# Kernel optimization log

Hardware: AMD Instinct MI355X
Metric: run time of the kernel (lower is better)

Reference implementation:

```python
import jax, jax.numpy as jnp
import numpy as np

EPS = 1e-8
EPS12 = 1e-12
TAU = 0.2
IOU_THRESHOLD = 0.5
NEG_INF = -1e9

N, C = 8192, 1024
HID, FGD, CLSD = 256, 64, 128


def setup_inputs() -> dict:
    key = jax.random.key(0)
    ks = jax.random.split(key, 16)
    roi_feats = jax.random.normal(ks[0], (N, C), dtype=jnp.float32)
    # labels in {-1 (ignore), 0 (bg), 1..20 (classes)}
    labels = jax.random.randint(ks[1], (N,), 0, 21, dtype=jnp.int64) - 1
    ious = jax.random.uniform(ks[2], (N,), dtype=jnp.float32)
    s = 0.02
    w1f = jax.random.normal(ks[3], (HID, C), dtype=jnp.float32) * s
    b1f = jnp.zeros((HID,), dtype=jnp.float32)
    w2f = jax.random.normal(ks[4], (FGD, HID), dtype=jnp.float32) * s
    b2f = jnp.zeros((FGD,), dtype=jnp.float32)
    w1c = jax.random.normal(ks[5], (HID, C), dtype=jnp.float32) * s
    b1c = jnp.zeros((HID,), dtype=jnp.float32)
    w2c = jax.random.normal(ks[6], (CLSD, HID), dtype=jnp.float32) * s
    b2c = jnp.zeros((CLSD,), dtype=jnp.float32)
    return {"roi_feats": roi_feats, "labels": labels, "ious": ious,
            "w1f": w1f, "b1f": b1f, "w2f": w2f, "b2f": b2f,
            "w1c": w1c, "b1c": b1c, "w2c": w2c, "b2c": b2c}


def _project_normalize(x, w1, b1, w2, b2):
    h = jax.nn.relu(x @ w1.T + b1)
    z = h @ w2.T + b2
    nrm = jnp.linalg.norm(z, axis=1, keepdims=True)  # F.normalize: z / max(||z||, eps)
    return z / jnp.maximum(nrm, EPS)


def _fg_bg_loss(z_fg, fg_mask, ignore_mask, iou_weight):
    n = z_fg.shape[0]
    anchor = fg_mask & ~ignore_mask
    eye = jnp.eye(n, dtype=bool)
    # pos_mask[i,j] = fg_mask[j] & ~ignore[j], self excluded
    pos = (fg_mask & ~ignore_mask)[None, :] & ~eye  # [N,N]
    sim = (z_fg @ z_fg.T) / TAU
    sim_exp = jnp.exp(sim) * (~eye).astype(sim.dtype)
    denom = sim_exp.sum(axis=1)  # [N]
    numer = jnp.sum(jnp.exp(sim) * pos.astype(sim.dtype), axis=1)  # [N]
    n_pos = pos.sum(axis=1)
    loss_i = -jnp.log((numer + EPS) / (denom + EPS))
    valid = anchor & (n_pos > 0)
    w = iou_weight
    num = jnp.sum(jnp.where(valid, loss_i * w, 0.0))
    den = jnp.sum(jnp.where(valid, w, 0.0)) + EPS
    return num / den


def _class_supcon_loss(z_cls, labels, fg_mask, ignore_mask, iou_weight):
    n = z_cls.shape[0]
    anchor = fg_mask & ~ignore_mask
    eye = jnp.eye(n, dtype=bool)
    valid_den = ~eye & ~ignore_mask[None, :]  # [N,N]
    # pos[i,j]: same label, j not ignored, labels[j] != 0, j != i, j valid
    pos = (labels[None, :] == labels[:, None]) & ~ignore_mask[None, :] & (labels[None, :] != 0)
    pos = pos & ~eye & valid_den
    sim = (z_cls @ z_cls.T) / TAU
    logits = jnp.where(valid_den, sim, NEG_INF)
    denom_log = jax.nn.logsumexp(logits, axis=1)  # [N]
    n_pos = pos.sum(axis=1)
    sum_pos = jnp.sum(jnp.where(pos, sim, 0.0), axis=1)
    n_pos_safe = jnp.maximum(n_pos, 1).astype(sim.dtype)
    loss_i = -(sum_pos - n_pos.astype(sim.dtype) * denom_log) / n_pos_safe
    valid = anchor & (n_pos > 0) & valid_den.any(axis=1)
    w = iou_weight
    num = jnp.sum(jnp.where(valid, loss_i * w, 0.0))
    den = jnp.sum(jnp.where(valid, w, 0.0)) + EPS12
    return num / den


def reference(roi_feats, labels, ious, w1f, b1f, w2f, b2f, w1c, b1c, w2c, b2c):
    z_fg = _project_normalize(roi_feats, w1f, b1f, w2f, b2f)
    z_cls = _project_normalize(roi_feats, w1c, b1c, w2c, b2c)
    ignore_mask = labels == -1
    bg_mask = (labels == 0) & ~ignore_mask
    fg_mask = (labels > 0) & ~ignore_mask
    iou_weight = jnp.where(ious > IOU_THRESHOLD, ious, 0.0)
    loss_fg_bg = _fg_bg_loss(z_fg, fg_mask, ignore_mask, iou_weight)
    loss_supcon = _class_supcon_loss(z_cls, labels, fg_mask, ignore_mask, iou_weight)
    # loss_weights = (1.0, 1.0); stacked as [loss_fg_bg, loss_supcon]
    return jnp.stack([loss_fg_bg * 1.0, loss_supcon * 1.0])
```

## Files before the change

kernel.cpp:

```cpp
#include <hip/hip_runtime.h>
#include <hip/hip_bf16.h>
#include <math.h>

#define N_ROI 8192
#define C_IN  1024
#define HIDD  256
#define FGD   64
#define CLSD  128
#define INV_TAU 5.0f

using frag_ab = __attribute__((ext_vector_type(8))) short;
using f32x16  = __attribute__((ext_vector_type(16))) float;

static __device__ __forceinline__ short f32_to_bf16_bits(float f) {
  unsigned u = __builtin_bit_cast(unsigned, f);
  u = (u + 0x7FFFu + ((u >> 16) & 1u)) >> 16;
  return (short)u;
}
static __device__ __forceinline__ float bf16_bits_to_f32(short b) {
  unsigned u = ((unsigned)(unsigned short)b) << 16;
  return __builtin_bit_cast(float, u);
}

__global__ void prep_zero_kernel(float* accum, int* cnt) {
  int t = threadIdx.x;
  if (t < 8) accum[t] = 0.f;
  if (t < 24) cnt[t] = 0;
}

__global__ void prep_stats_kernel(const int* __restrict__ labels,
                                  float* __restrict__ Sfg, float* __restrict__ Pfg,
                                  float* __restrict__ Scls, float* __restrict__ SPc,
                                  float* __restrict__ pfv, float* __restrict__ nimv,
                                  float* __restrict__ ljmv, int* __restrict__ cnt) {
  int i = blockIdx.x * blockDim.x + threadIdx.x;
  if (i >= N_ROI) return;
  Sfg[i] = 0.f; Pfg[i] = 0.f; Scls[i] = 0.f; SPc[i] = 0.f;
  int l = labels[i];
  pfv[i]  = (l > 0)  ? 1.f : 0.f;
  nimv[i] = (l != -1) ? 1.f : 0.f;
  ljmv[i] = (l > 0)  ? (float)l : -7.f;
  int b = l + 1; if (b < 0) b = 0; if (b > 21) b = 21;
  atomicAdd(&cnt[b], 1);
}

__global__ __launch_bounds__(256) void pack_w_kernel(
    const float* __restrict__ w1f, const float* __restrict__ w1c,
    const float* __restrict__ w2f, const float* __restrict__ w2c,
    short* __restrict__ W1pf, short* __restrict__ W1pc,
    short* __restrict__ W2pf, short* __restrict__ W2pc) {
  int b = blockIdx.x;
  const float* src; short* dst; int Ksh; int b0;
  if (b < 128)      { src = w1f; dst = W1pf; Ksh = 10; b0 = 0; }
  else if (b < 256) { src = w1c; dst = W1pc; Ksh = 10; b0 = 128; }
  else if (b < 264) { src = w2f; dst = W2pf; Ksh = 8;  b0 = 256; }
  else              { src = w2c; dst = W2pc; Ksh = 8;  b0 = 264; }
  int K = 1 << Ksh;
  int f = (b - b0) * 256 + threadIdx.x;
  int r = f >> (Ksh - 3);
  int c0 = (f & ((K >> 3) - 1)) << 3;
  float4 v0 = *(const float4*)(src + (size_t)r * K + c0);
  float4 v1 = *(const float4*)(src + (size_t)r * K + c0 + 4);
  union { short s[8]; uint4 v; } o;
  o.s[0] = f32_to_bf16_bits(v0.x); o.s[1] = f32_to_bf16_bits(v0.y);
  o.s[2] = f32_to_bf16_bits(v0.z); o.s[3] = f32_to_bf16_bits(v0.w);
  o.s[4] = f32_to_bf16_bits(v1.x); o.s[5] = f32_to_bf16_bits(v1.y);
  o.s[6] = f32_to_bf16_bits(v1.z); o.s[7] = f32_to_bf16_bits(v1.w);
  ((uint4*)dst)[(size_t)((r >> 5) * (K >> 4) + (c0 >> 4)) * 64 +
                ((c0 >> 3) & 1) * 32 + (r & 31)] = o.v;
}

__global__ __launch_bounds__(256) void gemm1_kernel(
    const float* __restrict__ X,
    const short* __restrict__ W1pf, const short* __restrict__ W1pc,
    const float* __restrict__ b1f, const float* __restrict__ b1c,
    short* __restrict__ Hpf, short* __restrict__ Hpc) {
  __shared__ union {
    short stageA[2][1024];
    short T[4][128 * 36];
  } sm;
  int tid = threadIdx.x, lane = tid & 63, wv = tid >> 6;
  int Mb = blockIdx.x;
  const short* Wp = (wv >> 1) ? W1pc : W1pf;
  const float* b1 = (wv >> 1) ? b1c  : b1f;
  short*       Hp = (wv >> 1) ? Hpc  : Hpf;
  const uint4* Wv4 = (const uint4*)Wp;
  int arow = tid >> 3;
  int ac4  = tid & 7;
  const float* Xp = X + (size_t)(Mb * 32 + arow) * C_IN + ac4 * 4;
  int aslot = ((ac4 >> 2) * 64 + ((ac4 >> 1) & 1) * 32 + arow) * 8 + (ac4 & 1) * 4;

  float4 av;
  frag_ab breg[2][8];
  f32x16 acc[4];
  #pragma unroll
  for (int nt = 0; nt < 4; ++nt)
    #pragma unroll
    for (int q = 0; q < 16; ++q) acc[nt][q] = 0.f;

  auto loadA = [&](int c) { av = *(const float4*)(Xp + c * 32); };
  auto loadB = [&](int c, int s) {
    #pragma unroll
    for (int kci = 0; kci < 2; ++kci)
      #pragma unroll
      for (int nt = 0; nt < 4; ++nt)
        breg[s][kci * 4 + nt] =
            *(const frag_ab*)&Wv4[(size_t)(((wv & 1) * 4 + nt) * 64 + c * 2 + kci) * 64 + lane];
  };
  auto storeA = [&](int buf) {
    *(short4*)&sm.stageA[buf][aslot] =
        make_short4(f32_to_bf16_bits(av.x), f32_to_bf16_bits(av.y),
                    f32_to_bf16_bits(av.z), f32_to_bf16_bits(av.w));
  };
  auto domfma = [&](int buf, int bank) {
    frag_ab a0 = *(const frag_ab*)&sm.stageA[buf][(0 * 64 + lane) * 8];
    frag_ab a1 = *(const frag_ab*)&sm.stageA[buf][(1 * 64 + lane) * 8];
    #pragma unroll
    for (int nt = 0; nt < 4; ++nt)
      acc[nt] = __builtin_amdgcn_mfma_f32_32x32x16_bf16(a0, breg[bank][nt], acc[nt], 0, 0, 0);
    #pragma unroll
    for (int nt = 0; nt < 4; ++nt)
      acc[nt] = __builtin_amdgcn_mfma_f32_32x32x16_bf16(a1, breg[bank][4 + nt], acc[nt], 0, 0, 0);
  };

  loadA(0); loadB(0, 0); storeA(0);
  __syncthreads();
  for (int c = 0; c < 32; c += 2) {
    if (c + 1 < 32) { loadA(c + 1); loadB(c + 1, 1); }
    domfma(0, 0);
    if (c + 1 < 32) storeA(1);
    __syncthreads();
    if (c + 2 < 32) { loadA(c + 2); loadB(c + 2, 0); }
    domfma(1, 1);
    if (c + 2 < 32) storeA(0);
    __syncthreads();
  }
  int cl31 = lane & 31, h = lane >> 5;
  short* T = sm.T[wv];
  #pragma unroll
  for (int nt = 0; nt < 4; ++nt) {
    int colLocal = nt * 32 + cl31;
    float bb = b1[(wv & 1) * 128 + colLocal];
    #pragma unroll
    for (int g = 0; g < 4; ++g) {
      float x0 = fmaxf(acc[nt][g * 4 + 0] + bb, 0.f);
      float x1 = fmaxf(acc[nt][g * 4 + 1] + bb, 0.f);
      float x2 = fmaxf(acc[nt][g * 4 + 2] + bb, 0.f);
      float x3 = fmaxf(acc[nt][g * 4 + 3] + bb, 0.f);
      *(short4*)&T[colLocal * 36 + 4 * h + 8 * g] =
          make_short4(f32_to_bf16_bits(x0), f32_to_bf16_bits(x1),
                      f32_to_bf16_bits(x2), f32_to_bf16_bits(x3));
    }
  }
  __syncthreads();
  uint4* Hv4 = (uint4*)Hp;
  #pragma unroll
  for (int k = 0; k < 8; ++k) {
    union { short s[8]; uint4 v; } o;
    int c0 = k * 16 + h * 8;
    #pragma unroll
    for (int e = 0; e < 8; ++e) o.s[e] = T[(c0 + e) * 36 + cl31];
    Hv4[(size_t)(Mb * 16 + (wv & 1) * 8 + k) * 64 + h * 32 + cl31] = o.v;
  }
}

template<int D>
__device__ __forceinline__ void gemm2_head(
    const short* __restrict__ Hp, const short* __restrict__ W2p,
    const float* __restrict__ b2, short* __restrict__ Zr,
    float* __restrict__ tii, short* __restrict__ T, int gt) {
  int lane = threadIdx.x & 63;
  const frag_ab* Hv = (const frag_ab*)Hp;
  const frag_ab* Wv = (const frag_ab*)W2p;
  constexpr int NT = D / 32;
  frag_ab a[16];
  #pragma unroll
  for (int kc = 0; kc < 16; ++kc) a[kc] = Hv[(size_t)(gt * 16 + kc) * 64 + lane];
  f32x16 acc[NT];
  #pragma unroll
  for (int j = 0; j < NT; ++j)
    #pragma unroll
    for (int q = 0; q < 16; ++q) acc[j][q] = 0.f;
  #pragma unroll
  for (int kc = 0; kc < 16; ++kc)
    #pragma unroll
    for (int j = 0; j < NT; ++j)
      acc[j] = __builtin_amdgcn_mfma_f32_32x32x16_bf16(a[kc], Wv[(j * 16 + kc) * 64 + lane], acc[j], 0, 0, 0);
  int c = lane & 31, h = lane >> 5;
  float bb[NT];
  #pragma unroll
  for (int j = 0; j < NT; ++j) bb[j] = b2[j * 32 + c];
  float s1[16];
  #pragma unroll
  for (int r = 0; r < 16; ++r) {
    s1[r] = 0.f;
    #pragma unroll
    for (int j = 0; j < NT; ++j) {
      float v = acc[j][r] + bb[j];
      s1[r] += v * v;
    }
  }
  #pragma unroll
  for (int r = 0; r < 16; ++r)
    #pragma unroll
    for (int m = 1; m < 32; m <<= 1) s1[r] += __shfl_xor(s1[r], m);
  float s2[16];
  #pragma unroll
  for (int r = 0; r < 16; ++r) s2[r] = 0.f;
  #pragma unroll
  for (int j = 0; j < NT; ++j) {
    int cl = j * 32 + c;
    #pragma unroll
    for (int g = 0; g < 4; ++g) {
      short q0, q1, q2, q3;
      #pragma unroll
      for (int e = 0; e < 4; ++e) {
        int r = g * 4 + e;
        float sc = 1.f / fmaxf(sqrtf(s1[r]), 1e-8f);
        short qb = f32_to_bf16_bits((acc[j][r] + bb[j]) * sc);
        float zf = bf16_bits_to_f32(qb);
        s2[r] += zf * zf;
        if (e == 0) q0 = qb; else if (e == 1) q1 = qb; else if (e == 2) q2 = qb; else q3 = qb;
      }
      *(short4*)&T[cl * 36 + 4 * h + 8 * g] = make_short4(q0, q1, q2, q3);
    }
  }
  #pragma unroll
  for (int r = 0; r < 16; ++r)
    #pragma unroll
    for (int m = 1; m < 32; m <<= 1) s2[r] += __shfl_xor(s2[r], m);
  if (c == 0) {
    #pragma unroll
    for (int r = 0; r < 16; ++r)
      tii[gt * 32 + (r & 3) + 8 * (r >> 2) + 4 * h] = s2[r];
  }
  __syncthreads();
  uint4* Zv = (uint4*)Zr;
  #pragma unroll
  for (int k = 0; k < D / 16; ++k) {
    int c0 = (2 * k + h) * 8;
    union { short s[8]; uint4 u; } o;
    #pragma unroll
    for (int e = 0; e < 8; ++e) o.s[e] = T[(c0 + e) * 36 + c];
    Zv[(size_t)(gt * (D / 16) + k) * 64 + h * 32 + c] = o.u;
  }
}

__global__ __launch_bounds__(128) void gemm2_kernel(
    const short* __restrict__ Hpf, const short* __restrict__ Hpc,
    const short* __restrict__ W2pf, const short* __restrict__ W2pc,
    const float* __restrict__ b2f, const float* __restrict__ b2c,
    short* __restrict__ Zrf, short* __restrict__ Zrc,
    float* __restrict__ tiif, float* __restrict__ tiic) {
  __shared__ short T2[2][128 * 36];
  int wv = threadIdx.x >> 6;
  int b = blockIdx.x;
  if (b < 128)
    gemm2_head<64>(Hpf, W2pf, b2f, Zrf, tiif, T2[wv], b * 2 + wv);
  else
    gemm2_head<128>(Hpc, W2pc, b2c, Zrc, tiic, T2[wv], (b - 128) * 2 + wv);
}

template<int D, int MODE, int NJT>
__device__ __forceinline__ void loss_body(
    short* sbuf, const short* __restrict__ Zr, const int* __restrict__ labels,
    const float* __restrict__ pfv, const float* __restrict__ nimv,
    const float* __restrict__ ljmv,
    float* __restrict__ Sg, float* __restrict__ Pg) {
  constexpr int KC = D / 16;
  int tid = threadIdx.x, lane = tid & 63, wv = tid >> 6;
  int itile = blockIdx.x * 4 + wv;
  const frag_ab* Zrv = (const frag_ab*)Zr;
  frag_ab a[KC];
  #pragma unroll
  for (int kc = 0; kc < KC; ++kc) a[kc] = Zrv[(itile * KC + kc) * 64 + lane];
  float limf[16];
  if (MODE == 1) {
    #pragma unroll
    for (int r = 0; r < 16; ++r) {
      int row = (r & 3) + 8 * (r >> 2) + 4 * (lane >> 5);
      limf[r] = (float)labels[itile * 32 + row];
    }
  }
  float Ssum[16] = {}, Psum[16] = {};
  int jt0 = blockIdx.y * NJT;
  {
    const uint4* src = (const uint4*)(Zr + (size_t)jt0 * KC * 512);
    uint4* dst = (uint4*)sbuf;
    #pragma unroll
    for (int q = 0; q < KC * 64; q += 256) dst[q + tid] = src[q + tid];
  }
  __syncthreads();
  for (int kk = 0; kk < NJT; ++kk) {
    int jt = jt0 + kk;
    if (kk + 1 < NJT) {
      const uint4* src = (const uint4*)(Zr + (size_t)(jt + 1) * KC * 512);
      uint4* dst = (uint4*)(sbuf + ((kk + 1) & 1) * KC * 512);
      #pragma unroll
      for (int q = 0; q < KC * 64; q += 256) dst[q + tid] = src[q + tid];
    }
    const frag_ab* bvf = (const frag_ab*)(sbuf + (kk & 1) * KC * 512);
    int j = jt * 32 + (lane & 31);
    float pf = 0.f, nim = 0.f, ljm = 0.f;
    if (MODE == 0) pf = pfv[j];
    else { nim = nimv[j]; ljm = ljmv[j]; }
    f32x16 acc;
    #pragma unroll
    for (int q = 0; q < 16; ++q) acc[q] = 0.f;
    #pragma unroll
    for (int kc = 0; kc < KC; ++kc)
      acc = __builtin_amdgcn_mfma_f32_32x32x16_bf16(a[kc], bvf[kc * 64 + lane], acc, 0, 0, 0);
    #pragma unroll
    for (int r = 0; r < 16; ++r) {
      if (MODE == 0) {
        float e = __expf(acc[r] * INV_TAU);
        Ssum[r] += e;
        Psum[r] = fmaf(pf, e, Psum[r]);
      } else {
        float t = acc[r] * INV_TAU;
        float e = __expf(t);
        Ssum[r] = fmaf(nim, e, Ssum[r]);
        Psum[r] += (limf[r] == ljm) ? t : 0.f;
      }
    }
    __syncthreads();
  }
  #pragma unroll
  for (int r = 0; r < 16; ++r) {
    float s = Ssum[r], p = Psum[r];
    #pragma unroll
    for (int m = 1; m < 32; m <<= 1) { s += __shfl_xor(s, m); p += __shfl_xor(p, m); }
    if ((lane & 31) == 0) {
      int row = (r & 3) + 8 * (r >> 2) + 4 * (lane >> 5);
      atomicAdd(&Sg[itile * 32 + row], s);
      atomicAdd(&Pg[itile * 32 + row], p);
    }
  }
}

__global__ __launch_bounds__(256) void loss_kernel(
    const short* __restrict__ Zrf, const short* __restrict__ Zrc,
    const int* __restrict__ labels,
    const float* __restrict__ pfv, const float* __restrict__ nimv,
    const float* __restrict__ ljmv,
    float* __restrict__ Sfg, float* __restrict__ Pfg,
    float* __restrict__ Scls, float* __restrict__ SPc) {
  __shared__ __align__(16) short sbuf[2 * 8 * 512];
  if (blockIdx.z == 0)
    loss_body<FGD, 0, 16>(sbuf, Zrf, labels, pfv, nimv, ljmv, Sfg, Pfg);
  else
    loss_body<CLSD, 1, 16>(sbuf, Zrc, labels, pfv, nimv, ljmv, Scls, SPc);
}

__global__ __launch_bounds__(256) void finalize_kernel(
    const float* __restrict__ Sfg, const float* __restrict__ Pfg,
    const float* __restrict__ Scls, const float* __restrict__ SPc,
    const float* __restrict__ tiif, const float* __restrict__ tiic,
    const int* __restrict__ labels, const float* __restrict__ ious,
    int* __restrict__ cnt, float* __restrict__ accum, float* __restrict__ out) {
  int i = blockIdx.x * 256 + threadIdx.x;
  int l = labels[i];
  float iv = ious[i];
  float w = (iv > 0.5f) ? iv : 0.f;
  int cntP = 0;
  #pragma unroll
  for (int b = 2; b <= 21; ++b) cntP += cnt[b];
  int cntNI = N_ROI - cnt[0];
  bool Pi = (l > 0);
  float numF = 0.f, denF = 0.f, numC = 0.f, denC = 0.f;
  float eF = __expf(INV_TAU * tiif[i]);
  float Sf = Sfg[i] - eF;
  float Pf = Pfg[i] - (Pi ? eF : 0.f);
  int nposF = cntP - (Pi ? 1 : 0);
  if (Pi && nposF > 0) {
    float lossF = logf((Sf + 1e-8f) / (Pf + 1e-8f));
    numF = lossF * w; denF = w;
  }
  float tC = INV_TAU * tiic[i];
  float eC = __expf(tC);
  float Sc = Scls[i] - ((l != -1) ? eC : 0.f);
  float SP = SPc[i] - (Pi ? tC : 0.f);
  int nposC = Pi ? (cnt[l + 1] - 1) : 0;
  bool anyv = (cntNI - ((l != -1) ? 1 : 0)) > 0;
  if (Pi && nposC > 0 && anyv) {
    float lse = logf(Sc);
    float lossC = -(SP - (float)nposC * lse) / fmaxf((float)nposC, 1.f);
    numC = lossC * w; denC = w;
  }
  float v0 = numF, v1 = denF, v2 = numC, v3 = denC;
  #pragma unroll
  for (int m = 1; m < 64; m <<= 1) {
    v0 += __shfl_xor(v0, m); v1 += __shfl_xor(v1, m);
    v2 += __shfl_xor(v2, m); v3 += __shfl_xor(v3, m);
  }
  __shared__ float red[4][4];
  int lane = threadIdx.x & 63, wid = threadIdx.x >> 6;
  if (lane == 0) { red[wid][0]=v0; red[wid][1]=v1; red[wid][2]=v2; red[wid][3]=v3; }
  __syncthreads();
  if (threadIdx.x == 0) {
    float s0=0,s1=0,s2=0,s3=0;
    for (int q = 0; q < 4; ++q) { s0+=red[q][0]; s1+=red[q][1]; s2+=red[q][2]; s3+=red[q][3]; }
    atomicAdd(&accum[0], s0); atomicAdd(&accum[1], s1);
    atomicAdd(&accum[2], s2); atomicAdd(&accum[3], s3);
    __threadfence();
    int t = atomicAdd(&cnt[22], 1);
    if (t == 31) {
      __threadfence();
      out[0] = accum[0] / (accum[1] + 1e-8f);
      out[1] = accum[2] / (accum[3] + 1e-12f);
    }
  }
}

extern "C" void kernel_launch(void* const* d_in, const int* in_sizes, int n_in,
                              void* d_out, int out_size, void* d_ws, size_t ws_size,
                              hipStream_t stream) {
  const float* X    = (const float*)d_in[0];
  const int*  labels= (const int*)d_in[1];
  const float* ious = (const float*)d_in[2];
  const float* w1f  = (const float*)d_in[3];
  const float* b1f  = (const float*)d_in[4];
  const float* w2f  = (const float*)d_in[5];
  const float* b2f  = (const float*)d_in[6];
  const float* w1c  = (const float*)d_in[7];
  const float* b1c  = (const float*)d_in[8];
  const float* w2c  = (const float*)d_in[9];
  const float* b2c  = (const float*)d_in[10];
  float* out = (float*)d_out;

  char* w = (char*)d_ws;
  short* W1pf = (short*)w;            w += 524288;
  short* W1pc = (short*)w;            w += 524288;
  short* W2pf = (short*)w;            w += 32768;
  short* W2pc = (short*)w;            w += 65536;
  short* Hpf  = (short*)w;            w += 4194304;
  short* Hpc  = (short*)w;            w += 4194304;
  short* Zrf  = (short*)w;            w += 1048576;
  short* Zrc  = (short*)w;            w += 2097152;
  float* Sfg  = (float*)w;            w += 32768;
  float* Pfg  = (float*)w;            w += 32768;
  float* Scls = (float*)w;            w += 32768;
  float* SPc  = (float*)w;            w += 32768;
  float* tiif = (float*)w;            w += 32768;
  float* tiic = (float*)w;            w += 32768;
  float* pfv  = (float*)w;            w += 32768;
  float* nimv = (float*)w;            w += 32768;
  float* ljmv = (float*)w;            w += 32768;
  float* accum= (float*)w;            w += 32;
  int*   cnt  = (int*)w;              w += 96;

  prep_zero_kernel<<<1, 64, 0, stream>>>(accum, cnt);
  prep_stats_kernel<<<N_ROI/256, 256, 0, stream>>>(labels, Sfg, Pfg, Scls, SPc,
                                                   pfv, nimv, ljmv, cnt);
  pack_w_kernel<<<280, 256, 0, stream>>>(w1f, w1c, w2f, w2c, W1pf, W1pc, W2pf, W2pc);

  gemm1_kernel<<<256, 256, 0, stream>>>(X, W1pf, W1pc, b1f, b1c, Hpf, Hpc);
  gemm2_kernel<<<256, 128, 0, stream>>>(Hpf, Hpc, W2pf, W2pc, b2f, b2c,
                                        Zrf, Zrc, tiif, tiic);

  loss_kernel<<<dim3(64, 16, 2), 256, 0, stream>>>(Zrf, Zrc, labels, pfv, nimv, ljmv,
                                                   Sfg, Pfg, Scls, SPc);

  finalize_kernel<<<N_ROI/256, 256, 0, stream>>>(Sfg, Pfg, Scls, SPc, tiif, tiic,
                                                 labels, ious, cnt, accum, out);
}
```

Before: 209.4 us.

## Fold temperature and log2e into A operand and load B tiles directly into registers

The loss kernel now pre-scales the anchor fragments by 1/tau·log2(e) once, so each similarity exponent becomes a bare exp2 with no multiply. The positive-similarity sum is rescaled by ln2 at the end. The shared-memory staging of B tiles and its per-tile barriers are dropped in favour of register double-buffering loaded straight from global/L2, along with a fully unrolled j loop. The extra bf16 rounding of the pre-scaled A changes numerics slightly, and the register buffers raise VGPR pressure while each wave now fetches B tiles redundantly.

```diff
diff --git a/kernel.cpp b/kernel.cpp
--- a/kernel.cpp
+++ b/kernel.cpp
@@ -8,6 +8,8 @@
 #define FGD   64
 #define CLSD  128
 #define INV_TAU 5.0f
+#define SCALE_LOG2E 7.2134752f
+#define LN2F 0.69314718f
 
 using frag_ab = __attribute__((ext_vector_type(8))) short;
 using f32x16  = __attribute__((ext_vector_type(16))) float;
@@ -20,6 +22,13 @@
 static __device__ __forceinline__ float bf16_bits_to_f32(short b) {
   unsigned u = ((unsigned)(unsigned short)b) << 16;
   return __builtin_bit_cast(float, u);
+}
+static __device__ __forceinline__ float fast_exp2(float x) {
+#if __has_builtin(__builtin_amdgcn_exp2f)
+  return __builtin_amdgcn_exp2f(x);
+#else
+  return exp2f(x);
+#endif
 }
 
 __global__ void prep_zero_kernel(float* accum, int* cnt) {
@@ -263,7 +272,7 @@
 
 template<int D, int MODE, int NJT>
 __device__ __forceinline__ void loss_body(
-    short* sbuf, const short* __restrict__ Zr, const int* __restrict__ labels,
+    const short* __restrict__ Zr, const int* __restrict__ labels,
     const float* __restrict__ pfv, const float* __restrict__ nimv,
     const float* __restrict__ ljmv,
     float* __restrict__ Sg, float* __restrict__ Pg) {
@@ -273,7 +282,13 @@
   const frag_ab* Zrv = (const frag_ab*)Zr;
   frag_ab a[KC];
   #pragma unroll
-  for (int kc = 0; kc < KC; ++kc) a[kc] = Zrv[(itile * KC + kc) * 64 + lane];
+  for (int kc = 0; kc < KC; ++kc) {
+    frag_ab t = Zrv[(itile * KC + kc) * 64 + lane];
+    #pragma unroll
+    for (int e = 0; e < 8; ++e)
+      t[e] = f32_to_bf16_bits(bf16_bits_to_f32(t[e]) * SCALE_LOG2E);
+    a[kc] = t;
+  }
   float limf[16];
   if (MODE == 1) {
     #pragma unroll
@@ -284,46 +299,41 @@
   }
   float Ssum[16] = {}, Psum[16] = {};
   int jt0 = blockIdx.y * NJT;
-  {
-    const uint4* src = (const uint4*)(Zr + (size_t)jt0 * KC * 512);
-    uint4* dst = (uint4*)sbuf;
-    #pragma unroll
-    for (int q = 0; q < KC * 64; q += 256) dst[q + tid] = src[q + tid];
-  }
-  __syncthreads();
+  int jlane = lane & 31;
+
+  frag_ab bb[2][KC];
+  float pfb[2], nimb[2], ljmb[2];
+  auto loadB = [&](int bank, int jt) {
+    #pragma unroll
+    for (int kc = 0; kc < KC; ++kc)
+      bb[bank][kc] = Zrv[((size_t)jt * KC + kc) * 64 + lane];
+    int j = jt * 32 + jlane;
+    if (MODE == 0) pfb[bank] = pfv[j];
+    else { nimb[bank] = nimv[j]; ljmb[bank] = ljmv[j]; }
+  };
+
+  loadB(0, jt0);
+  #pragma unroll
   for (int kk = 0; kk < NJT; ++kk) {
-    int jt = jt0 + kk;
-    if (kk + 1 < NJT) {
-      const uint4* src = (const uint4*)(Zr + (size_t)(jt + 1) * KC * 512);
-      uint4* dst = (uint4*)(sbuf + ((kk + 1) & 1) * KC * 512);
-      #pragma unroll
-      for (int q = 0; q < KC * 64; q += 256) dst[q + tid] = src[q + tid];
-    }
-    const frag_ab* bvf = (const frag_ab*)(sbuf + (kk & 1) * KC * 512);
-    int j = jt * 32 + (lane & 31);
-    float pf = 0.f, nim = 0.f, ljm = 0.f;
-    if (MODE == 0) pf = pfv[j];
-    else { nim = nimv[j]; ljm = ljmv[j]; }
+    int bank = kk & 1;
+    if (kk + 1 < NJT) loadB(bank ^ 1, jt0 + kk + 1);
     f32x16 acc;
     #pragma unroll
     for (int q = 0; q < 16; ++q) acc[q] = 0.f;
     #pragma unroll
     for (int kc = 0; kc < KC; ++kc)
-      acc = __builtin_amdgcn_mfma_f32_32x32x16_bf16(a[kc], bvf[kc * 64 + lane], acc, 0, 0, 0);
+      acc = __builtin_amdgcn_mfma_f32_32x32x16_bf16(a[kc], bb[bank][kc], acc, 0, 0, 0);
     #pragma unroll
     for (int r = 0; r < 16; ++r) {
+      float e = fast_exp2(acc[r]);
       if (MODE == 0) {
-        float e = __expf(acc[r] * INV_TAU);
         Ssum[r] += e;
-        Psum[r] = fmaf(pf, e, Psum[r]);
+        Psum[r] = fmaf(pfb[bank], e, Psum[r]);
       } else {
-        float t = acc[r] * INV_TAU;
-        float e = __expf(t);
-        Ssum[r] = fmaf(nim, e, Ssum[r]);
-        Psum[r] += (limf[r] == ljm) ? t : 0.f;
+        Ssum[r] = fmaf(nimb[bank], e, Ssum[r]);
+        Psum[r] += (limf[r] == ljmb[bank]) ? acc[r] : 0.f;
       }
     }
-    __syncthreads();
   }
   #pragma unroll
   for (int r = 0; r < 16; ++r) {
@@ -331,6 +341,7 @@
     #pragma unroll
     for (int m = 1; m < 32; m <<= 1) { s += __shfl_xor(s, m); p += __shfl_xor(p, m); }
     if ((lane & 31) == 0) {
+      if (MODE == 1) p *= LN2F;
       int row = (r & 3) + 8 * (r >> 2) + 4 * (lane >> 5);
       atomicAdd(&Sg[itile * 32 + row], s);
       atomicAdd(&Pg[itile * 32 + row], p);
@@ -345,11 +356,10 @@
     const float* __restrict__ ljmv,
     float* __restrict__ Sfg, float* __restrict__ Pfg,
     float* __restrict__ Scls, float* __restrict__ SPc) {
-  __shared__ __align__(16) short sbuf[2 * 8 * 512];
   if (blockIdx.z == 0)
-    loss_body<FGD, 0, 16>(sbuf, Zrf, labels, pfv, nimv, ljmv, Sfg, Pfg);
+    loss_body<FGD, 0, 16>(Zrf, labels, pfv, nimv, ljmv, Sfg, Pfg);
   else
-    loss_body<CLSD, 1, 16>(sbuf, Zrc, labels, pfv, nimv, ljmv, Scls, SPc);
+    loss_body<CLSD, 1, 16>(Zrc, labels, pfv, nimv, ljmv, Scls, SPc);
 }
 
 __global__ __launch_bounds__(256) void finalize_kernel(
```

Result: slower. 287.4 us (+37.3%).
